# Kernel optimization log

Measured on AMD Instinct MI355X. Metric: run time of the kernel, lower is better.

Reference implementation:

```python
import jax, jax.numpy as jnp
import numpy as np

B, S, E, H = 4, 2048, 1024, 16
DK = E // H  # 64


def setup_inputs() -> dict:
    key = jax.random.key(0)
    ks = jax.random.split(key, 12)
    sc_in = 1.0 / np.sqrt(E)
    sc_dk = 1.0 / np.sqrt(DK)
    inp = {
        "Q": jax.random.normal(ks[0], (B, S, E), jnp.float32),
        "K": jax.random.normal(ks[1], (B, S, E), jnp.float32),
        "V": jax.random.normal(ks[2], (B, S, E), jnp.float32),
        # per-head projection weights, torch Linear layout [out, in] stacked over heads
        "Wq": jax.random.normal(ks[3], (H, DK, E), jnp.float32) * sc_in,
        "bq": jax.random.normal(ks[4], (H, DK), jnp.float32) * sc_in,
        "Wk": jax.random.normal(ks[5], (H, DK, E), jnp.float32) * sc_in,
        "bk": jax.random.normal(ks[6], (H, DK), jnp.float32) * sc_in,
        "Wv": jax.random.normal(ks[7], (H, DK, E), jnp.float32) * sc_in,
        "bv": jax.random.normal(ks[8], (H, DK), jnp.float32) * sc_in,
        # output projection (intended embed_dim -> embed_dim)
        "Wo": jax.random.normal(ks[9], (E, E), jnp.float32) * sc_in,
        "bo": jax.random.normal(ks[10], (E,), jnp.float32) * sc_in,
    }
    return inp


def reference(Q, K, V, Wq, bq, Wk, bk, Wv, bv, Wo, bo):
    scale = 1.0 / jnp.sqrt(jnp.asarray(DK, Q.dtype))
    # per-head linear projections (vectorized over heads): [B,H,S,DK]
    q = jnp.einsum("bse,hde->bhsd", Q, Wq) + bq[None, :, None, :]
    k = jnp.einsum("bse,hde->bhsd", K, Wk) + bk[None, :, None, :]
    v = jnp.einsum("bse,hde->bhsd", V, Wv) + bv[None, :, None, :]
    # scaled dot-product attention (no mask, dropout=0.0)
    scores = jnp.einsum("bhsd,bhtd->bhst", q, k) * scale  # [B,H,S,S]
    attn = jax.nn.softmax(scores, axis=-1)
    ctx = jnp.einsum("bhst,bhtd->bhsd", attn, v)  # [B,H,S,DK]
    # concat heads along feature dim -> [B,S,E]
    ctx = ctx.transpose(0, 2, 1, 3).reshape(B, S, E)
    return ctx @ Wo.T + bo
```

## Files before the change

### kernel.cpp

```cpp
#include <hip/hip_runtime.h>
#include <stdint.h>

typedef __attribute__((ext_vector_type(8))) short vs8;
typedef __attribute__((ext_vector_type(4))) short vs4;
typedef __attribute__((ext_vector_type(4))) float vf4;

#define DEV static __device__ __forceinline__

DEV unsigned short f2bf(float x){
  union { float f; uint32_t u; } v; v.f = x;
  uint32_t r = v.u + 0x7fffu + ((v.u >> 16) & 1u);
  return (unsigned short)(r >> 16);
}

DEV void gload_lds16(const void* g, void* l){
  __builtin_amdgcn_global_load_lds((const __attribute__((address_space(1))) void*)g,
                                   (__attribute__((address_space(3))) void*)l, 16, 0, 0);
}

__global__ void cvt_w(const float* __restrict__ s, unsigned short* __restrict__ d, int n){
  int i = (blockIdx.x * blockDim.x + threadIdx.x) * 4;
  if (i >= n) return;
  vf4 f = *reinterpret_cast<const vf4*>(s + i);
  vs4 o;
  o[0] = (short)f2bf(f[0]); o[1] = (short)f2bf(f[1]);
  o[2] = (short)f2bf(f[2]); o[3] = (short)f2bf(f[3]);
  *reinterpret_cast<vs4*>(d + i) = o;
}


DEV void stage_f32(const float* __restrict__ g, long row0, int K, int kt,
                   unsigned short* lds, int tid){
  int r_ = tid >> 3, c = tid & 7;
#pragma unroll
  for (int i = 0; i < 4; ++i){
    int row = i*32 + r_;
    const float* src = g + (row0 + row) * (long)K + kt + c*8;
    vf4 f0 = *reinterpret_cast<const vf4*>(src);
    vf4 f1 = *reinterpret_cast<const vf4*>(src + 4);
    vs8 p;
    p[0]=(short)f2bf(f0[0]); p[1]=(short)f2bf(f0[1]); p[2]=(short)f2bf(f0[2]); p[3]=(short)f2bf(f0[3]);
    p[4]=(short)f2bf(f1[0]); p[5]=(short)f2bf(f1[1]); p[6]=(short)f2bf(f1[2]); p[7]=(short)f2bf(f1[3]);
    int slot = c ^ (row & 7);
    *reinterpret_cast<vs8*>(&lds[row*64 + slot*8]) = p;
  }
}

DEV void stage_bf16(const unsigned short* __restrict__ g, long row0, int K, int kt,
                    unsigned short* lds, int lane, int wid){
#pragma unroll
  for (int i = 0; i < 4; ++i){
    int stripe = wid*32 + i*8;
    int row = stripe + (lane >> 3);
    int chunk = (lane & 7) ^ (row & 7);
    const unsigned short* src = g + (row0 + row) * (long)K + kt + chunk*8;
    gload_lds16(src, &lds[stripe*64]);
  }
}

DEV vs8 lds_frag(const unsigned short* lds, int row, int slot){
  return *reinterpret_cast<const vs8*>(&lds[row*64 + (slot ^ (row & 7))*8]);
}

template<int A_F32, int B_F32, int OUT_F32, int BIAS_ROW>
__global__ __launch_bounds__(256)
void gemm_bt(const void* __restrict__ Ap, const void* __restrict__ Bp,
             const float* __restrict__ bias, void* __restrict__ Cp,
             int M, int N, int K, float oscale, long aB, long bB, long cB)
{
  __shared__ unsigned short As[128*64];
  __shared__ unsigned short Bs[128*64];
  const int tid = threadIdx.x, lane = tid & 63, wid = tid >> 6;
  const int nt = N >> 7, mt = M >> 7;
  int idx = blockIdx.x;
  const int per = mt * nt;
  const int batch = idx / per; idx -= batch * per;
  const long m0 = (long)(idx / nt) * 128;
  const long n0 = (long)(idx % nt) * 128;
  const int wm = (wid >> 1) * 64, wn = (wid & 1) * 64;
  const int cl = lane & 15, gr = lane >> 4;

  vf4 acc[4][4] = {};

  for (int kt = 0; kt < K; kt += 64){
    if (A_F32) stage_f32((const float*)Ap + aB*batch, m0, K, kt, As, tid);
    else       stage_bf16((const unsigned short*)Ap + aB*batch, m0, K, kt, As, lane, wid);
    if (B_F32) stage_f32((const float*)Bp + bB*batch, n0, K, kt, Bs, tid);
    else       stage_bf16((const unsigned short*)Bp + bB*batch, n0, K, kt, Bs, lane, wid);
    __syncthreads();
#pragma unroll
    for (int ks = 0; ks < 2; ++ks){
      vs8 af[4], bf[4];
#pragma unroll
      for (int mi = 0; mi < 4; ++mi) af[mi] = lds_frag(As, wm + mi*16 + cl, ks*4 + gr);
#pragma unroll
      for (int ni = 0; ni < 4; ++ni) bf[ni] = lds_frag(Bs, wn + ni*16 + cl, ks*4 + gr);
#pragma unroll
      for (int mi = 0; mi < 4; ++mi)
#pragma unroll
        for (int ni = 0; ni < 4; ++ni)
          acc[mi][ni] = __builtin_amdgcn_mfma_f32_16x16x32_bf16(af[mi], bf[ni], acc[mi][ni], 0, 0, 0);
    }
    __syncthreads();
  }

#pragma unroll
  for (int mi = 0; mi < 4; ++mi)
#pragma unroll
    for (int ni = 0; ni < 4; ++ni)
#pragma unroll
      for (int r = 0; r < 4; ++r){
        long m = m0 + wm + mi*16 + gr*4 + r;
        long n = n0 + wn + ni*16 + cl;
        float v = (acc[mi][ni][r] + (BIAS_ROW ? bias[m] : bias[n])) * oscale;
        if (OUT_F32) (((float*)Cp) + cB*batch)[m*(long)N + n] = v;
        else (((unsigned short*)Cp) + cB*batch)[m*(long)N + n] = f2bf(v);
      }
}

__global__ __launch_bounds__(256)
void attn_kernel(const unsigned short* __restrict__ qg, const unsigned short* __restrict__ kg,
                 const unsigned short* __restrict__ vg, unsigned short* __restrict__ og)
{
  __shared__ __align__(16) unsigned short Ks[2][32*64];
  __shared__ __align__(16) unsigned short Vs[2][4*64*8];
  __shared__ __align__(16) unsigned short Pl[4][16*40];
  const int tid = threadIdx.x, lane = tid & 63, wid = tid >> 6;
  const int cl = lane & 15, gr = lane >> 4;
  const int bid = blockIdx.x;
  const int qb = bid & 31, h = (bid >> 5) & 15, b = bid >> 9;
  const int s0 = qb*64 + wid*16;

  const unsigned short* qp = qg + ((long)(b*2048 + s0 + cl))*1024 + h*64 + gr*8;
  vs8 q0 = *(const vs8*)(qp);
  vs8 q1 = *(const vs8*)(qp + 32);

  const unsigned short* kb = kg + ((long)b*2048)*1024 + h*64;
  const unsigned short* vb = vg + ((long)(b*1024) + h*64)*2048;

  vf4 o0 = {}, o1 = {}, o2 = {}, o3 = {};
  float m = -__builtin_inff(), lsum = 0.f;

  const int krow = tid >> 3, ksl = tid & 7;
  const int vd = tid >> 2, vsl = tid & 3;
  unsigned short* ldsK0 = &Ks[0][(tid & 192)*8];
  unsigned short* ldsK1 = &Ks[1][(tid & 192)*8];
  unsigned short* Pw = Pl[wid];

  gload_lds16(kb + (long)krow*1024 + ((ksl ^ (krow & 7))*8), ldsK0);
  {
    vs8 vr = *(const vs8*)(vb + (long)vd*2048 + vsl*8);
    *(vs8*)(&Vs[0][(vsl*64 + vd)*8]) = vr;
  }
  __syncthreads();

  int cur = 0;
  for (int j0 = 0; j0 < 2048; j0 += 32){
    const int more = (j0 + 32) < 2048;
    vs8 vr;
    if (more){
      gload_lds16(kb + (long)(j0 + 32 + krow)*1024 + ((ksl ^ (krow & 7))*8),
                  cur ? ldsK0 : ldsK1);
      vr = *(const vs8*)(vb + (long)vd*2048 + (j0 + 32) + vsl*8);
    }
    const unsigned short* ksb = Ks[cur];
    const unsigned short* vsb = Vs[cur];

    vf4 sa = {}, sb = {};
    {
      vs8 a00 = lds_frag(ksb, cl,      gr);
      vs8 a01 = lds_frag(ksb, cl,      4 + gr);
      sa = __builtin_amdgcn_mfma_f32_16x16x32_bf16(a00, q0, sa, 0, 0, 0);
      sa = __builtin_amdgcn_mfma_f32_16x16x32_bf16(a01, q1, sa, 0, 0, 0);
      vs8 a10 = lds_frag(ksb, 16 + cl, gr);
      vs8 a11 = lds_frag(ksb, 16 + cl, 4 + gr);
      sb = __builtin_amdgcn_mfma_f32_16x16x32_bf16(a10, q0, sb, 0, 0, 0);
      sb = __builtin_amdgcn_mfma_f32_16x16x32_bf16(a11, q1, sb, 0, 0, 0);
    }
    float t = fmaxf(fmaxf(fmaxf(sa[0], sa[1]), fmaxf(sa[2], sa[3])),
                    fmaxf(fmaxf(sb[0], sb[1]), fmaxf(sb[2], sb[3])));
    t = fmaxf(t, __shfl_xor(t, 16));
    t = fmaxf(t, __shfl_xor(t, 32));
    float mn = fmaxf(m, t);
    float al = exp2f(m - mn);
    m = mn;
    lsum *= al;
#pragma unroll
    for (int r = 0; r < 4; ++r){ o0[r] *= al; o1[r] *= al; o2[r] *= al; o3[r] *= al; }
#pragma unroll
    for (int r = 0; r < 4; ++r){ sa[r] = exp2f(sa[r] - m); sb[r] = exp2f(sb[r] - m); }
    lsum += ((sa[0]+sa[1]) + (sa[2]+sa[3])) + ((sb[0]+sb[1]) + (sb[2]+sb[3]));

    int2 wa, wb;
    wa.x = (int)(unsigned)f2bf(sa[0]) | ((int)(unsigned)f2bf(sa[1]) << 16);
    wa.y = (int)(unsigned)f2bf(sa[2]) | ((int)(unsigned)f2bf(sa[3]) << 16);
    wb.x = (int)(unsigned)f2bf(sb[0]) | ((int)(unsigned)f2bf(sb[1]) << 16);
    wb.y = (int)(unsigned)f2bf(sb[2]) | ((int)(unsigned)f2bf(sb[3]) << 16);
    *reinterpret_cast<int2*>(&Pw[cl*40 + gr*4])      = wa;
    *reinterpret_cast<int2*>(&Pw[cl*40 + 16 + gr*4]) = wb;

    vs8 pa = *reinterpret_cast<const vs8*>(&Pw[cl*40 + gr*8]);

    o0 = __builtin_amdgcn_mfma_f32_16x16x32_bf16(*(const vs8*)(vsb + (gr*64 +  0 + cl)*8), pa, o0, 0, 0, 0);
    o1 = __builtin_amdgcn_mfma_f32_16x16x32_bf16(*(const vs8*)(vsb + (gr*64 + 16 + cl)*8), pa, o1, 0, 0, 0);
    o2 = __builtin_amdgcn_mfma_f32_16x16x32_bf16(*(const vs8*)(vsb + (gr*64 + 32 + cl)*8), pa, o2, 0, 0, 0);
    o3 = __builtin_amdgcn_mfma_f32_16x16x32_bf16(*(const vs8*)(vsb + (gr*64 + 48 + cl)*8), pa, o3, 0, 0, 0);

    if (more) *(vs8*)(&Vs[cur ^ 1][(vsl*64 + vd)*8]) = vr;
    __syncthreads();
    cur ^= 1;
  }

  float ls = lsum;
  ls += __shfl_xor(ls, 16);
  ls += __shfl_xor(ls, 32);
  float inv = 1.0f / ls;
  unsigned short* ob = og + ((long)(b*2048 + s0 + cl))*1024 + h*64 + gr*4;
  vs4 w0, w1, w2, w3;
#pragma unroll
  for (int r = 0; r < 4; ++r){
    w0[r] = (short)f2bf(o0[r] * inv);
    w1[r] = (short)f2bf(o1[r] * inv);
    w2[r] = (short)f2bf(o2[r] * inv);
    w3[r] = (short)f2bf(o3[r] * inv);
  }
  *(vs4*)(ob +  0) = w0;
  *(vs4*)(ob + 16) = w1;
  *(vs4*)(ob + 32) = w2;
  *(vs4*)(ob + 48) = w3;
}

extern "C" void kernel_launch(void* const* d_in, const int* in_sizes, int n_in,
                              void* d_out, int out_size, void* d_ws, size_t ws_size,
                              hipStream_t stream)
{
  (void)in_sizes; (void)n_in; (void)out_size; (void)ws_size;
  const float* Q  = (const float*)d_in[0];
  const float* K  = (const float*)d_in[1];
  const float* V  = (const float*)d_in[2];
  const float* bq = (const float*)d_in[4];
  const float* bk = (const float*)d_in[6];
  const float* bv = (const float*)d_in[8];
  const float* bo = (const float*)d_in[10];
  const float* Wq = (const float*)d_in[3];
  const float* Wk = (const float*)d_in[5];
  const float* Wv = (const float*)d_in[7];
  const float* Wo = (const float*)d_in[9];

  unsigned short* q   = (unsigned short*)d_ws;
  unsigned short* k   = q   + (size_t)8*1024*1024;
  unsigned short* vT  = k   + (size_t)8*1024*1024;
  unsigned short* ctx = vT  + (size_t)8*1024*1024;
  unsigned short* wqb = ctx + (size_t)8*1024*1024;
  unsigned short* wkb = wqb + (size_t)1024*1024;
  unsigned short* wvb = wkb + (size_t)1024*1024;
  unsigned short* wob = wvb + (size_t)1024*1024;

  const int WN = 1024*1024;
  cvt_w<<<1024, 256, 0, stream>>>(Wq, wqb, WN);
  cvt_w<<<1024, 256, 0, stream>>>(Wk, wkb, WN);
  cvt_w<<<1024, 256, 0, stream>>>(Wv, wvb, WN);
  cvt_w<<<1024, 256, 0, stream>>>(Wo, wob, WN);

  const float qscale = 0.125f * 1.4426950408889634f;

  gemm_bt<1,0,0,0><<<512, 256, 0, stream>>>(Q, wqb, bq, q, 8192, 1024, 1024, qscale, 0, 0, 0);
  gemm_bt<1,0,0,0><<<512, 256, 0, stream>>>(K, wkb, bk, k, 8192, 1024, 1024, 1.0f, 0, 0, 0);
  gemm_bt<0,1,0,1><<<512, 256, 0, stream>>>(wvb, V, bv, vT, 1024, 2048, 1024, 1.0f,
                                            0, (long)2048*1024, (long)1024*2048);
  attn_kernel<<<2048, 256, 0, stream>>>(q, k, vT, ctx);
  gemm_bt<0,0,1,0><<<512, 256, 0, stream>>>(ctx, wob, bo, d_out, 8192, 1024, 1024, 1.0f, 0, 0, 0);
}
```

Measured before the change: 478.6 us.

## Pre-convert activations to bf16, widen attention KV tile to 64, lazy rescale

Q, K and V are converted to bf16 by separate kernels into scratch space that reuses the ctx and output buffers. This lets every projection GEMM stage operands with direct global-to-LDS loads instead of converting fp32 in registers. The attention kernel now processes 64 keys per iteration instead of 32, which halves the number of barriers and loop trips. It also skips the online-softmax rescale unless the running max grows by more than 8, and packs bf16 with a hardware cvt_pk instruction and the fast exp2 builtin. The extra conversion passes add memory traffic, the lazy rescale lets exp values grow up to 2^8 before renormalising, and the larger tiles use more LDS.

```diff
diff --git a/kernel.cpp b/kernel.cpp
--- a/kernel.cpp
+++ b/kernel.cpp
@@ -16,6 +16,10 @@
 DEV void gload_lds16(const void* g, void* l){
   __builtin_amdgcn_global_load_lds((const __attribute__((address_space(1))) void*)g,
                                    (__attribute__((address_space(3))) void*)l, 16, 0, 0);
+}
+
+DEV int cvtpk(float lo, float hi_){
+  int r; asm("v_cvt_pk_bf16_f32 %0, %1, %2" : "=v"(r) : "v"(lo), "v"(hi_)); return r;
 }
 
 __global__ void cvt_w(const float* __restrict__ s, unsigned short* __restrict__ d, int n){
@@ -29,23 +33,6 @@
 }
 
 
-DEV void stage_f32(const float* __restrict__ g, long row0, int K, int kt,
-                   unsigned short* lds, int tid){
-  int r_ = tid >> 3, c = tid & 7;
-#pragma unroll
-  for (int i = 0; i < 4; ++i){
-    int row = i*32 + r_;
-    const float* src = g + (row0 + row) * (long)K + kt + c*8;
-    vf4 f0 = *reinterpret_cast<const vf4*>(src);
-    vf4 f1 = *reinterpret_cast<const vf4*>(src + 4);
-    vs8 p;
-    p[0]=(short)f2bf(f0[0]); p[1]=(short)f2bf(f0[1]); p[2]=(short)f2bf(f0[2]); p[3]=(short)f2bf(f0[3]);
-    p[4]=(short)f2bf(f1[0]); p[5]=(short)f2bf(f1[1]); p[6]=(short)f2bf(f1[2]); p[7]=(short)f2bf(f1[3]);
-    int slot = c ^ (row & 7);
-    *reinterpret_cast<vs8*>(&lds[row*64 + slot*8]) = p;
-  }
-}
-
 DEV void stage_bf16(const unsigned short* __restrict__ g, long row0, int K, int kt,
                     unsigned short* lds, int lane, int wid){
 #pragma unroll
@@ -62,9 +49,9 @@
   return *reinterpret_cast<const vs8*>(&lds[row*64 + (slot ^ (row & 7))*8]);
 }
 
-template<int A_F32, int B_F32, int OUT_F32, int BIAS_ROW>
+template<int OUT_F32, int BIAS_ROW>
 __global__ __launch_bounds__(256)
-void gemm_bt(const void* __restrict__ Ap, const void* __restrict__ Bp,
+void gemm_bt(const unsigned short* __restrict__ Ap, const unsigned short* __restrict__ Bp,
              const float* __restrict__ bias, void* __restrict__ Cp,
              int M, int N, int K, float oscale, long aB, long bB, long cB)
 {
@@ -83,10 +70,8 @@
   vf4 acc[4][4] = {};
 
   for (int kt = 0; kt < K; kt += 64){
-    if (A_F32) stage_f32((const float*)Ap + aB*batch, m0, K, kt, As, tid);
-    else       stage_bf16((const unsigned short*)Ap + aB*batch, m0, K, kt, As, lane, wid);
-    if (B_F32) stage_f32((const float*)Bp + bB*batch, n0, K, kt, Bs, tid);
-    else       stage_bf16((const unsigned short*)Bp + bB*batch, n0, K, kt, Bs, lane, wid);
+    stage_bf16(Ap + aB*batch, m0, K, kt, As, lane, wid);
+    stage_bf16(Bp + bB*batch, n0, K, kt, Bs, lane, wid);
     __syncthreads();
 #pragma unroll
     for (int ks = 0; ks < 2; ++ks){
@@ -122,9 +107,9 @@
 void attn_kernel(const unsigned short* __restrict__ qg, const unsigned short* __restrict__ kg,
                  const unsigned short* __restrict__ vg, unsigned short* __restrict__ og)
 {
-  __shared__ __align__(16) unsigned short Ks[2][32*64];
-  __shared__ __align__(16) unsigned short Vs[2][4*64*8];
-  __shared__ __align__(16) unsigned short Pl[4][16*40];
+  __shared__ __align__(16) unsigned short Ks[2][64*64];
+  __shared__ __align__(16) unsigned short Vs[2][8*64*8];
+  __shared__ __align__(16) unsigned short Pl[4][16*72];
   const int tid = threadIdx.x, lane = tid & 63, wid = tid >> 6;
   const int cl = lane & 15, gr = lane >> 4;
   const int bid = blockIdx.x;
@@ -141,72 +126,94 @@
   vf4 o0 = {}, o1 = {}, o2 = {}, o3 = {};
   float m = -__builtin_inff(), lsum = 0.f;
 
-  const int krow = tid >> 3, ksl = tid & 7;
+  const int krow = tid >> 3;
+  const int kchunk = ((tid & 7) ^ (krow & 7)) * 8;
   const int vd = tid >> 2, vsl = tid & 3;
-  unsigned short* ldsK0 = &Ks[0][(tid & 192)*8];
-  unsigned short* ldsK1 = &Ks[1][(tid & 192)*8];
+  const int kbase = (tid & 192) * 8;
   unsigned short* Pw = Pl[wid];
 
-  gload_lds16(kb + (long)krow*1024 + ((ksl ^ (krow & 7))*8), ldsK0);
+  gload_lds16(kb + (long)krow*1024 + kchunk,        &Ks[0][kbase]);
+  gload_lds16(kb + (long)(krow + 32)*1024 + kchunk, &Ks[0][32*64 + kbase]);
   {
-    vs8 vr = *(const vs8*)(vb + (long)vd*2048 + vsl*8);
-    *(vs8*)(&Vs[0][(vsl*64 + vd)*8]) = vr;
+    vs8 va = *(const vs8*)(vb + (long)vd*2048 + vsl*8);
+    vs8 vb2 = *(const vs8*)(vb + (long)vd*2048 + 32 + vsl*8);
+    *(vs8*)(&Vs[0][(vsl*64 + vd)*8]) = va;
+    *(vs8*)(&Vs[0][((vsl + 4)*64 + vd)*8]) = vb2;
   }
   __syncthreads();
 
   int cur = 0;
-  for (int j0 = 0; j0 < 2048; j0 += 32){
-    const int more = (j0 + 32) < 2048;
-    vs8 vr;
+  for (int j0 = 0; j0 < 2048; j0 += 64){
+    const int more = (j0 + 64) < 2048;
+    vs8 va, vb2;
     if (more){
-      gload_lds16(kb + (long)(j0 + 32 + krow)*1024 + ((ksl ^ (krow & 7))*8),
-                  cur ? ldsK0 : ldsK1);
-      vr = *(const vs8*)(vb + (long)vd*2048 + (j0 + 32) + vsl*8);
+      const long nj = j0 + 64;
+      gload_lds16(kb + (nj + krow)*1024 + kchunk,      &Ks[cur ^ 1][kbase]);
+      gload_lds16(kb + (nj + krow + 32)*1024 + kchunk, &Ks[cur ^ 1][32*64 + kbase]);
+      va  = *(const vs8*)(vb + (long)vd*2048 + nj + vsl*8);
+      vb2 = *(const vs8*)(vb + (long)vd*2048 + nj + 32 + vsl*8);
     }
     const unsigned short* ksb = Ks[cur];
     const unsigned short* vsb = Vs[cur];
 
-    vf4 sa = {}, sb = {};
-    {
-      vs8 a00 = lds_frag(ksb, cl,      gr);
-      vs8 a01 = lds_frag(ksb, cl,      4 + gr);
-      sa = __builtin_amdgcn_mfma_f32_16x16x32_bf16(a00, q0, sa, 0, 0, 0);
-      sa = __builtin_amdgcn_mfma_f32_16x16x32_bf16(a01, q1, sa, 0, 0, 0);
-      vs8 a10 = lds_frag(ksb, 16 + cl, gr);
-      vs8 a11 = lds_frag(ksb, 16 + cl, 4 + gr);
-      sb = __builtin_amdgcn_mfma_f32_16x16x32_bf16(a10, q0, sb, 0, 0, 0);
-      sb = __builtin_amdgcn_mfma_f32_16x16x32_bf16(a11, q1, sb, 0, 0, 0);
-    }
-    float t = fmaxf(fmaxf(fmaxf(sa[0], sa[1]), fmaxf(sa[2], sa[3])),
-                    fmaxf(fmaxf(sb[0], sb[1]), fmaxf(sb[2], sb[3])));
+    vf4 s[4];
+#pragma unroll
+    for (int jt = 0; jt < 4; ++jt){
+      vf4 z = {};
+      vs8 aA = lds_frag(ksb, jt*16 + cl, gr);
+      z = __builtin_amdgcn_mfma_f32_16x16x32_bf16(aA, q0, z, 0, 0, 0);
+      vs8 aB = lds_frag(ksb, jt*16 + cl, 4 + gr);
+      z = __builtin_amdgcn_mfma_f32_16x16x32_bf16(aB, q1, z, 0, 0, 0);
+      s[jt] = z;
+    }
+
+    float t0 = fmaxf(fmaxf(s[0][0], s[0][1]), fmaxf(s[0][2], s[0][3]));
+    float t1 = fmaxf(fmaxf(s[1][0], s[1][1]), fmaxf(s[1][2], s[1][3]));
+    float t2 = fmaxf(fmaxf(s[2][0], s[2][1]), fmaxf(s[2][2], s[2][3]));
+    float t3 = fmaxf(fmaxf(s[3][0], s[3][1]), fmaxf(s[3][2], s[3][3]));
+    float t = fmaxf(fmaxf(t0, t1), fmaxf(t2, t3));
     t = fmaxf(t, __shfl_xor(t, 16));
     t = fmaxf(t, __shfl_xor(t, 32));
-    float mn = fmaxf(m, t);
-    float al = exp2f(m - mn);
-    m = mn;
-    lsum *= al;
-#pragma unroll
-    for (int r = 0; r < 4; ++r){ o0[r] *= al; o1[r] *= al; o2[r] *= al; o3[r] *= al; }
-#pragma unroll
-    for (int r = 0; r < 4; ++r){ sa[r] = exp2f(sa[r] - m); sb[r] = exp2f(sb[r] - m); }
-    lsum += ((sa[0]+sa[1]) + (sa[2]+sa[3])) + ((sb[0]+sb[1]) + (sb[2]+sb[3]));
-
-    int2 wa, wb;
-    wa.x = (int)(unsigned)f2bf(sa[0]) | ((int)(unsigned)f2bf(sa[1]) << 16);
-    wa.y = (int)(unsigned)f2bf(sa[2]) | ((int)(unsigned)f2bf(sa[3]) << 16);
-    wb.x = (int)(unsigned)f2bf(sb[0]) | ((int)(unsigned)f2bf(sb[1]) << 16);
-    wb.y = (int)(unsigned)f2bf(sb[2]) | ((int)(unsigned)f2bf(sb[3]) << 16);
-    *reinterpret_cast<int2*>(&Pw[cl*40 + gr*4])      = wa;
-    *reinterpret_cast<int2*>(&Pw[cl*40 + 16 + gr*4]) = wb;
-
-    vs8 pa = *reinterpret_cast<const vs8*>(&Pw[cl*40 + gr*8]);
-
-    o0 = __builtin_amdgcn_mfma_f32_16x16x32_bf16(*(const vs8*)(vsb + (gr*64 +  0 + cl)*8), pa, o0, 0, 0, 0);
-    o1 = __builtin_amdgcn_mfma_f32_16x16x32_bf16(*(const vs8*)(vsb + (gr*64 + 16 + cl)*8), pa, o1, 0, 0, 0);
-    o2 = __builtin_amdgcn_mfma_f32_16x16x32_bf16(*(const vs8*)(vsb + (gr*64 + 32 + cl)*8), pa, o2, 0, 0, 0);
-    o3 = __builtin_amdgcn_mfma_f32_16x16x32_bf16(*(const vs8*)(vsb + (gr*64 + 48 + cl)*8), pa, o3, 0, 0, 0);
-
-    if (more) *(vs8*)(&Vs[cur ^ 1][(vsl*64 + vd)*8]) = vr;
+
+    if (__any(t > m + 8.f)){
+      float mn = fmaxf(m, t);
+      float al = __builtin_amdgcn_exp2f(m - mn);
+      m = mn; lsum *= al;
+#pragma unroll
+      for (int r = 0; r < 4; ++r){ o0[r] *= al; o1[r] *= al; o2[r] *= al; o3[r] *= al; }
+    }
+
+#pragma unroll
+    for (int jt = 0; jt < 4; ++jt)
+#pragma unroll
+      for (int r = 0; r < 4; ++r)
+        s[jt][r] = __builtin_amdgcn_exp2f(s[jt][r] - m);
+    lsum += (((s[0][0]+s[0][1]) + (s[0][2]+s[0][3])) + ((s[1][0]+s[1][1]) + (s[1][2]+s[1][3])))
+          + (((s[2][0]+s[2][1]) + (s[2][2]+s[2][3])) + ((s[3][0]+s[3][1]) + (s[3][2]+s[3][3])));
+
+#pragma unroll
+    for (int jt = 0; jt < 4; ++jt){
+      int2 w;
+      w.x = cvtpk(s[jt][0], s[jt][1]);
+      w.y = cvtpk(s[jt][2], s[jt][3]);
+      *reinterpret_cast<int2*>(&Pw[cl*72 + jt*16 + gr*4]) = w;
+    }
+    vs8 pa0 = *reinterpret_cast<const vs8*>(&Pw[cl*72 + gr*8]);
+    vs8 pa1 = *reinterpret_cast<const vs8*>(&Pw[cl*72 + 32 + gr*8]);
+
+    o0 = __builtin_amdgcn_mfma_f32_16x16x32_bf16(*(const vs8*)(vsb + (gr*64 +  0 + cl)*8), pa0, o0, 0, 0, 0);
+    o1 = __builtin_amdgcn_mfma_f32_16x16x32_bf16(*(const vs8*)(vsb + (gr*64 + 16 + cl)*8), pa0, o1, 0, 0, 0);
+    o2 = __builtin_amdgcn_mfma_f32_16x16x32_bf16(*(const vs8*)(vsb + (gr*64 + 32 + cl)*8), pa0, o2, 0, 0, 0);
+    o3 = __builtin_amdgcn_mfma_f32_16x16x32_bf16(*(const vs8*)(vsb + (gr*64 + 48 + cl)*8), pa0, o3, 0, 0, 0);
+    o0 = __builtin_amdgcn_mfma_f32_16x16x32_bf16(*(const vs8*)(vsb + ((4+gr)*64 +  0 + cl)*8), pa1, o0, 0, 0, 0);
+    o1 = __builtin_amdgcn_mfma_f32_16x16x32_bf16(*(const vs8*)(vsb + ((4+gr)*64 + 16 + cl)*8), pa1, o1, 0, 0, 0);
+    o2 = __builtin_amdgcn_mfma_f32_16x16x32_bf16(*(const vs8*)(vsb + ((4+gr)*64 + 32 + cl)*8), pa1, o2, 0, 0, 0);
+    o3 = __builtin_amdgcn_mfma_f32_16x16x32_bf16(*(const vs8*)(vsb + ((4+gr)*64 + 48 + cl)*8), pa1, o3, 0, 0, 0);
+
+    if (more){
+      *(vs8*)(&Vs[cur ^ 1][(vsl*64 + vd)*8]) = va;
+      *(vs8*)(&Vs[cur ^ 1][((vsl + 4)*64 + vd)*8]) = vb2;
+    }
     __syncthreads();
     cur ^= 1;
   }
@@ -256,18 +263,26 @@
   unsigned short* wvb = wkb + (size_t)1024*1024;
   unsigned short* wob = wvb + (size_t)1024*1024;
 
+  unsigned short* Qb = ctx;
+  unsigned short* Kb = (unsigned short*)d_out;
+  unsigned short* Vb = Kb + (size_t)8*1024*1024;
+
   const int WN = 1024*1024;
+  const int AN = 4*2048*1024;
   cvt_w<<<1024, 256, 0, stream>>>(Wq, wqb, WN);
   cvt_w<<<1024, 256, 0, stream>>>(Wk, wkb, WN);
   cvt_w<<<1024, 256, 0, stream>>>(Wv, wvb, WN);
   cvt_w<<<1024, 256, 0, stream>>>(Wo, wob, WN);
+  cvt_w<<<8192, 256, 0, stream>>>(Q, Qb, AN);
+  cvt_w<<<8192, 256, 0, stream>>>(K, Kb, AN);
+  cvt_w<<<8192, 256, 0, stream>>>(V, Vb, AN);
 
   const float qscale = 0.125f * 1.4426950408889634f;
 
-  gemm_bt<1,0,0,0><<<512, 256, 0, stream>>>(Q, wqb, bq, q, 8192, 1024, 1024, qscale, 0, 0, 0);
-  gemm_bt<1,0,0,0><<<512, 256, 0, stream>>>(K, wkb, bk, k, 8192, 1024, 1024, 1.0f, 0, 0, 0);
-  gemm_bt<0,1,0,1><<<512, 256, 0, stream>>>(wvb, V, bv, vT, 1024, 2048, 1024, 1.0f,
-                                            0, (long)2048*1024, (long)1024*2048);
+  gemm_bt<0,0><<<512, 256, 0, stream>>>(Qb, wqb, bq, q, 8192, 1024, 1024, qscale, 0, 0, 0);
+  gemm_bt<0,0><<<512, 256, 0, stream>>>(Kb, wkb, bk, k, 8192, 1024, 1024, 1.0f, 0, 0, 0);
+  gemm_bt<0,1><<<512, 256, 0, stream>>>(wvb, Vb, bv, vT, 1024, 2048, 1024, 1.0f,
+                                        0, (long)2048*1024, (long)1024*2048);
   attn_kernel<<<2048, 256, 0, stream>>>(q, k, vT, ctx);
-  gemm_bt<0,0,1,0><<<512, 256, 0, stream>>>(ctx, wob, bo, d_out, 8192, 1024, 1024, 1.0f, 0, 0, 0);
-}
+  gemm_bt<1,0><<<512, 256, 0, stream>>>(ctx, wob, bo, d_out, 8192, 1024, 1024, 1.0f, 0, 0, 0);
+}
```

Result: faster. 416.7 us (-12.9%).
